# Optimization experiments

Hardware: AMD Instinct MI355X
Metric: run time of the kernel (lower is better)

The kernel has to match this reference:

```python
import jax, jax.numpy as jnp
import numpy as np

BS, S, E, H = 64, 512, 1024, 16
HD = E // H
MASK_ID, KNOW_ID = 30001, 30002


def setup_inputs() -> dict:
    key = jax.random.key(0)
    ks = jax.random.split(key, 8)
    model_output = jax.random.normal(ks[0], (BS, S, E), dtype=jnp.float32)
    ids = jax.random.randint(ks[1], (BS, S), 0, 30000)  # never hits special ids
    ids = ids.at[:, 0].set(MASK_ID)        # exactly one [MASK] per sequence
    ids = ids.at[:, 1:9].set(KNOW_ID)      # 8 knowledge slots per sequence
    knowledge_output = jax.random.normal(ks[2], (BS, E), dtype=jnp.float32)
    empty_knowledge_mask = jax.random.randint(ks[3], (BS,), 0, 2).astype(bool)
    bound = 1.0 / np.sqrt(E)
    in_proj_weight = jax.random.uniform(ks[4], (3 * E, E), minval=-bound, maxval=bound, dtype=jnp.float32)
    in_proj_bias = jnp.zeros((3 * E,), jnp.float32)
    out_proj_weight = jax.random.uniform(ks[5], (E, E), minval=-bound, maxval=bound, dtype=jnp.float32)
    out_proj_bias = jnp.zeros((E,), jnp.float32)
    attention_strength = jnp.float32(0.1)
    return {
        "model_output": model_output,
        "knowledge_output": knowledge_output,
        "in_proj_weight": in_proj_weight,
        "in_proj_bias": in_proj_bias,
        "out_proj_weight": out_proj_weight,
        "out_proj_bias": out_proj_bias,
        "attention_strength": attention_strength,
        "input_ids": ids,
        "empty_knowledge_mask": empty_knowledge_mask,
        "knowledge_token_id": KNOW_ID,
        "mask_token_id": MASK_ID,
    }


def reference(model_output, knowledge_output, in_proj_weight, in_proj_bias,
              out_proj_weight, out_proj_bias, attention_strength,
              input_ids, empty_knowledge_mask, knowledge_token_id, mask_token_id):
    bs, sent_len, hidden = model_output.shape
    # --- knowledge injection: scatter knowledge vector into knowledge-token slots ---
    knowledge_mask = input_ids == knowledge_token_id                 # [bs, S]
    kv_src = jnp.where(knowledge_mask[:, :, None],
                       knowledge_output[:, None, :], model_output)  # [bs, S, E]
    # --- single-query gather: one [MASK] position per sequence ---
    mask_pos = jnp.argmax(input_ids == mask_token_id, axis=1)        # [bs]
    q_in = jnp.take_along_axis(kv_src, mask_pos[:, None, None], axis=1)[:, 0, :]  # [bs, E]
    # --- nn.MultiheadAttention (eval mode, dropout=0) ---
    Wq, Wk, Wv = in_proj_weight[:E], in_proj_weight[E:2 * E], in_proj_weight[2 * E:]
    bq, bk, bv = in_proj_bias[:E], in_proj_bias[E:2 * E], in_proj_bias[2 * E:]
    q = (q_in @ Wq.T + bq).reshape(bs, H, HD)                        # [bs, H, hd]
    k = (kv_src @ Wk.T + bk).reshape(bs, sent_len, H, HD)            # [bs, S, H, hd]
    v = (kv_src @ Wv.T + bv).reshape(bs, sent_len, H, HD)
    scale = 1.0 / np.sqrt(HD)
    scores = jnp.einsum('bhd,bshd->bhs', q * scale, k)               # [bs, H, S]
    attn = jax.nn.softmax(scores, axis=-1)
    ctx = jnp.einsum('bhs,bshd->bhd', attn, v).reshape(bs, hidden)   # [bs, E]
    attn_output = ctx @ out_proj_weight.T + out_proj_bias            # [bs, E]
    # --- residual on the ORIGINAL (pre-injection) mask-token states ---
    origin_q = jnp.take_along_axis(model_output, mask_pos[:, None, None], axis=1)[:, 0, :]
    mask_output = origin_q + attention_strength * attn_output
    # --- conditional restore where knowledge is empty ---
    mask_output = jnp.where(empty_knowledge_mask[:, None], origin_q, mask_output)
    return mask_output
```

## Files before the change

### kernel.cpp

```cpp
#include <hip/hip_runtime.h>

#define BS 64
#define S  512
#define E  1024
#define H  16
#define HD 64
#define SCALE 0.125f
#define CATT 8

#define W_QIN  1024
#define W_QKBF 66560
#define W_NUM  1115136
#define W_DEN  9503744
#define W_CTX  9511936

typedef __attribute__((ext_vector_type(8))) short short8;
typedef __attribute__((ext_vector_type(4))) float floatx4;

__device__ __forceinline__ unsigned int pack_bf16(float a, float b) {
    unsigned int ua = __float_as_uint(a), ub = __float_as_uint(b);
    ua = (ua + 0x7fffu + ((ua >> 16) & 1u)) >> 16;
    ub = (ub + 0x7fffu + ((ub >> 16) & 1u)) >> 16;
    return ua | (ub << 16);
}

__device__ __forceinline__ void fma4(float4& acc, float s, const float4& v) {
    acc.x += s * v.x; acc.y += s * v.y; acc.z += s * v.z; acc.w += s * v.w;
}
__device__ __forceinline__ float dot4(const float4& a, const float4& b) {
    return a.x * b.x + a.y * b.y + a.z * b.z + a.w * b.w;
}
__device__ __forceinline__ void bfly8(float* a) {
    #pragma unroll
    for (int off = 32; off > 0; off >>= 1) {
        #pragma unroll
        for (int i = 0; i < 8; i++) a[i] += __shfl_xor(a[i], off, 64);
    }
}

__global__ void k_prep(const float* __restrict__ model, const float* __restrict__ knowledge,
                       const int* __restrict__ ids, const int* __restrict__ mask_id_p,
                       const int* __restrict__ kid_p, int* __restrict__ mp,
                       float* __restrict__ qin) {
    int b = blockIdx.x, tid = threadIdx.x;
    __shared__ int best;
    if (tid == 0) best = S;
    __syncthreads();
    int mid = mask_id_p[0];
    for (int s = tid; s < S; s += 256)
        if (ids[b * S + s] == mid) atomicMin(&best, s);
    __syncthreads();
    int m = (best == S) ? 0 : best;
    if (tid == 0) mp[b] = m;
    bool isk = (ids[b * S + m] == kid_p[0]);
    const float* qrow = isk ? knowledge + (size_t)b * E : model + ((size_t)(b * S + m)) * E;
    ((float4*)(qin + (size_t)b * E))[tid] = ((const float4*)qrow)[tid];
}

__global__ void k_qgen(const float* __restrict__ qin, const float* __restrict__ w_in,
                       const float* __restrict__ b_in, unsigned short* __restrict__ qkbf) {
    int h = blockIdx.x, b0 = blockIdx.y * 4, t = threadIdx.x;
    __shared__ float qin_l[4][1024];
    __shared__ float qred[4][64][4];
    __shared__ float qs_l[4][64];
    #pragma unroll
    for (int k = 0; k < 4; k++) {
        int idx4 = k * 256 + t;
        int bb = idx4 >> 8, col = (idx4 & 255) * 4;
        *(float4*)&qin_l[bb][col] = *(const float4*)(qin + (size_t)(b0 + bb) * E + col);
    }
    __syncthreads();
    {
        int d = t >> 2, part = t & 3;
        const float* wr = w_in + (size_t)(h * HD + d) * E + part * 256;
        float acc[4] = {0.f, 0.f, 0.f, 0.f};
        for (int i = 0; i < 64; i++) {
            float4 wv = *(const float4*)(wr + i * 4);
            #pragma unroll
            for (int bb = 0; bb < 4; bb++)
                acc[bb] += dot4(wv, *(const float4*)&qin_l[bb][part * 256 + i * 4]);
        }
        #pragma unroll
        for (int bb = 0; bb < 4; bb++) qred[bb][d][part] = acc[bb];
    }
    __syncthreads();
    if (t < 64) {
        float bias = b_in[h * HD + t];
        #pragma unroll
        for (int bb = 0; bb < 4; bb++)
            qs_l[bb][t] = qred[bb][t][0] + qred[bb][t][1] + qred[bb][t][2] + qred[bb][t][3] + bias;
    }
    __syncthreads();
    {
        int e0 = t * 4;
        const float* wk = w_in + (size_t)(E + h * HD) * E + e0;
        float4 acc[4];
        #pragma unroll
        for (int bb = 0; bb < 4; bb++) acc[bb] = make_float4(0.f, 0.f, 0.f, 0.f);
        for (int d = 0; d < HD; d++) {
            float4 wv = *(const float4*)(wk + (size_t)d * E);
            #pragma unroll
            for (int bb = 0; bb < 4; bb++) fma4(acc[bb], qs_l[bb][d], wv);
        }
        #pragma unroll
        for (int bb = 0; bb < 4; bb++) {
            uint2 pk;
            pk.x = pack_bf16(acc[bb].x * SCALE, acc[bb].y * SCALE);
            pk.y = pack_bf16(acc[bb].z * SCALE, acc[bb].w * SCALE);
            *(uint2*)&qkbf[((size_t)(b0 + bb) * H + h) * E + e0] = pk;
        }
    }
}

__global__ __launch_bounds__(512, 4) void k_attn(
    const float* __restrict__ model, const float* __restrict__ knowledge,
    const int* __restrict__ ids, const int* __restrict__ kid_p,
    const unsigned short* __restrict__ qkbf, float* __restrict__ num, float* __restrict__ den) {
    __shared__ unsigned short Rbuf[16 * 1032];
    __shared__ unsigned short Pbuf[16 * 40];
    __shared__ const float* rowp[64];
    int tid = threadIdx.x;
    int l = tid & 63, w = tid >> 6;
    int quad = l >> 4, lm = l & 15;
    int c = blockIdx.x, b = blockIdx.y;
    int s0 = c * 64;
    if (tid < 64) {
        int id = ids[b * S + s0 + tid];
        rowp[tid] = (id == kid_p[0]) ? knowledge + (size_t)b * E
                                     : model + ((size_t)(b * S + s0 + tid)) * E;
    }
    const unsigned short* qh = qkbf + ((size_t)b * H + lm) * E;
    floatx4 accn[8];
    #pragma unroll
    for (int i = 0; i < 8; i++) accn[i] = (floatx4)0.f;
    float accden = 0.f;
    int ebw = w * 8;
    __syncthreads();

    for (int pass = 0; pass < 4; pass++) {
        int rbase = pass * 16;
        #pragma unroll
        for (int k = 0; k < 8; k++) {
            int row = 2 * k + (tid >> 8);
            const float* rp = rowp[rbase + row];
            int col = (tid & 255) * 4;
            float4 v = *(const float4*)(rp + col);
            uint2 pk;
            pk.x = pack_bf16(v.x, v.y);
            pk.y = pack_bf16(v.z, v.w);
            *(uint2*)&Rbuf[row * 1032 + col] = pk;
        }
        __syncthreads();
        if (w == 0) {
            floatx4 accs = (floatx4)0.f;
            for (int kk = 0; kk < 32; kk++) {
                short8 a = *(const short8*)(const void*)&Rbuf[lm * 1032 + kk * 32 + quad * 8];
                short8 bf = *(const short8*)(const void*)(qh + kk * 32 + quad * 8);
                accs = __builtin_amdgcn_mfma_f32_16x16x32_bf16(a, bf, accs, 0, 0, 0);
            }
            float e0 = __expf(accs[0]), e1 = __expf(accs[1]);
            float e2 = __expf(accs[2]), e3 = __expf(accs[3]);
            float sum = e0 + e1 + e2 + e3;
            sum += __shfl_xor(sum, 16, 64);
            sum += __shfl_xor(sum, 32, 64);
            accden += sum;
            uint2 pw;
            pw.x = pack_bf16(e0, e1);
            pw.y = pack_bf16(e2, e3);
            *(uint2*)&Pbuf[lm * 40 + quad * 4] = pw;
        }
        __syncthreads();
        short8 afr = {};
        if (quad < 2) afr = *(const short8*)(const void*)&Pbuf[lm * 40 + quad * 8];
        #pragma unroll
        for (int i = 0; i < 8; i++) {
            int e = (ebw + i) * 16 + lm;
            short8 bfr = {};
            if (quad < 2) {
                #pragma unroll
                for (int j = 0; j < 8; j++)
                    bfr[j] = (short)Rbuf[(quad * 8 + j) * 1032 + e];
            }
            accn[i] = __builtin_amdgcn_mfma_f32_16x16x32_bf16(afr, bfr, accn[i], 0, 0, 0);
        }
        __syncthreads();
    }
    size_t base = ((size_t)(c * BS + b) * H) * E;
    #pragma unroll
    for (int i = 0; i < 8; i++) {
        int e = (ebw + i) * 16 + lm;
        num[base + (size_t)(quad * 4 + 0) * E + e] = accn[i][0];
        num[base + (size_t)(quad * 4 + 1) * E + e] = accn[i][1];
        num[base + (size_t)(quad * 4 + 2) * E + e] = accn[i][2];
        num[base + (size_t)(quad * 4 + 3) * E + e] = accn[i][3];
    }
    if (w == 0 && l < 16) den[(size_t)(c * BS + b) * H + l] = accden;
}

__global__ void k_pc(const float* __restrict__ num, const float* __restrict__ den,
                     const float* __restrict__ w_in, const float* __restrict__ b_in,
                     float* __restrict__ ctx) {
    int h = blockIdx.x, b0 = blockIdx.y * 4, t = threadIdx.x;
    __shared__ float p_l[4][1024];
    __shared__ float cred[4][64][4];
    __shared__ float inv_l[4];
    #pragma unroll
    for (int k = 0; k < 4; k++) {
        int idx4 = k * 256 + t;
        int bb = idx4 >> 8, e4 = (idx4 & 255) * 4;
        float4 a = make_float4(0.f, 0.f, 0.f, 0.f);
        for (int cc = 0; cc < CATT; cc++) {
            float4 v = *(const float4*)(num + (((size_t)(cc * BS + b0 + bb) * H + h) * E) + e4);
            a.x += v.x; a.y += v.y; a.z += v.z; a.w += v.w;
        }
        *(float4*)&p_l[bb][e4] = a;
    }
    if (t < 4) {
        float ds = 0.f;
        for (int cc = 0; cc < CATT; cc++) ds += den[(size_t)(cc * BS + b0 + t) * H + h];
        inv_l[t] = 1.0f / ds;
    }
    __syncthreads();
    {
        int jj = t >> 2, part = t & 3;
        const float* wr = w_in + (size_t)(2 * E + h * HD + jj) * E + part * 256;
        float acc[4] = {0.f, 0.f, 0.f, 0.f};
        for (int i = 0; i < 64; i++) {
            float4 wv = *(const float4*)(wr + i * 4);
            #pragma unroll
            for (int bb = 0; bb < 4; bb++)
                acc[bb] += dot4(wv, *(const float4*)&p_l[bb][part * 256 + i * 4]);
        }
        #pragma unroll
        for (int bb = 0; bb < 4; bb++) cred[bb][jj][part] = acc[bb];
    }
    __syncthreads();
    if (t < 64) {
        float bias = b_in[2 * E + h * HD + t];
        #pragma unroll
        for (int bb = 0; bb < 4; bb++) {
            float s = cred[bb][t][0] + cred[bb][t][1] + cred[bb][t][2] + cred[bb][t][3];
            ctx[(size_t)(b0 + bb) * E + h * HD + t] = inv_l[bb] * s + bias;
        }
    }
}

__global__ void k_out(const float* __restrict__ model, const float* __restrict__ w_out,
                      const float* __restrict__ b_out, const float* __restrict__ ctx,
                      const int* __restrict__ mp, const int* __restrict__ empty,
                      const float* __restrict__ strength_p, float* __restrict__ out) {
    int w = threadIdx.x >> 6, l = threadIdx.x & 63;
    int j = blockIdx.x * 4 + w;
    int b0 = blockIdx.y * 8;
    const float* wr = w_out + (size_t)j * E;
    float4 wv[4];
    #pragma unroll
    for (int r = 0; r < 4; r++) wv[r] = *(const float4*)(wr + r * 256 + l * 4);
    float acc[8];
    #pragma unroll
    for (int bb = 0; bb < 8; bb++) {
        const float* src = ctx + (size_t)(b0 + bb) * E;
        float a = 0.f;
        #pragma unroll
        for (int r = 0; r < 4; r++) a += dot4(wv[r], *(const float4*)(src + r * 256 + l * 4));
        acc[bb] = a;
    }
    bfly8(acc);
    if (l < 8) {
        float myacc = acc[0];
        #pragma unroll
        for (int bb = 1; bb < 8; bb++) myacc = (l == bb) ? acc[bb] : myacc;
        int b = b0 + l;
        int m = mp[b];
        float orig = model[((size_t)(b * S + m)) * E + j];
        float bias = b_out[j];
        float st = strength_p[0];
        out[(size_t)b * E + j] = empty[b] ? orig : orig + st * (myacc + bias);
    }
}

extern "C" void kernel_launch(void* const* d_in, const int* in_sizes, int n_in,
                              void* d_out, int out_size, void* d_ws, size_t ws_size,
                              hipStream_t stream) {
    const float* model     = (const float*)d_in[0];
    const float* knowledge = (const float*)d_in[1];
    const float* w_in      = (const float*)d_in[2];
    const float* b_in      = (const float*)d_in[3];
    const float* w_out     = (const float*)d_in[4];
    const float* b_out     = (const float*)d_in[5];
    const float* strength  = (const float*)d_in[6];
    const int*   ids       = (const int*)d_in[7];
    const int*   empty     = (const int*)d_in[8];
    const int*   know_id   = (const int*)d_in[9];
    const int*   mask_id   = (const int*)d_in[10];
    float* out = (float*)d_out;

    float* ws  = (float*)d_ws;
    int*   mp  = (int*)d_ws;
    float* qin = ws + W_QIN;
    unsigned short* qkbf = (unsigned short*)(ws + W_QKBF);
    float* num = ws + W_NUM;
    float* den = ws + W_DEN;
    float* ctx = ws + W_CTX;

    k_prep<<<BS, 256, 0, stream>>>(model, knowledge, ids, mask_id, know_id, mp, qin);
    k_qgen<<<dim3(H, 16), 256, 0, stream>>>(qin, w_in, b_in, qkbf);
    k_attn<<<dim3(CATT, BS), 512, 0, stream>>>(model, knowledge, ids, know_id, qkbf, num, den);
    k_pc<<<dim3(H, 16), 256, 0, stream>>>(num, den, w_in, b_in, ctx);
    k_out<<<dim3(256, 8), 256, 0, stream>>>(model, w_out, b_out, ctx, mp, empty, strength, out);
}
```

Measured before the change: 284.1 us.

## Split score MFMA across waves, add transposed LDS tile, coalesce num stores

The attention kernel now builds both a row-major bf16 tile and a transposed copy in LDS so the P·V MFMA B-fragments load as two 8-byte reads instead of eight strided scalar reads. The QK score reduction is spread over four waves with a shared-memory partial-sum reduction instead of one wave doing all 32 MFMAs. Knowledge-row selection uses a ballot bitmask instead of a pointer table, and numerator results are staged through LDS to be written with coalesced float4 stores. This costs much more LDS per block, which may reduce occupancy, and the global loads become scalar per thread rather than float4.

```diff
diff --git a/kernel.cpp b/kernel.cpp
--- a/kernel.cpp
+++ b/kernel.cpp
@@ -17,13 +17,15 @@
 typedef __attribute__((ext_vector_type(8))) short short8;
 typedef __attribute__((ext_vector_type(4))) float floatx4;
 
+union S8u { uint2 u2[2]; short8 s; };
+
+__device__ __forceinline__ unsigned short bf16c(float x) {
+    unsigned int u = __float_as_uint(x);
+    return (unsigned short)((u + 0x7fffu + ((u >> 16) & 1u)) >> 16);
+}
 __device__ __forceinline__ unsigned int pack_bf16(float a, float b) {
-    unsigned int ua = __float_as_uint(a), ub = __float_as_uint(b);
-    ua = (ua + 0x7fffu + ((ua >> 16) & 1u)) >> 16;
-    ub = (ub + 0x7fffu + ((ub >> 16) & 1u)) >> 16;
-    return ua | (ub << 16);
-}
-
+    return (unsigned int)bf16c(a) | ((unsigned int)bf16c(b) << 16);
+}
 __device__ __forceinline__ void fma4(float4& acc, float s, const float4& v) {
     acc.x += s * v.x; acc.y += s * v.y; acc.z += s * v.z; acc.w += s * v.w;
 }
@@ -116,57 +118,89 @@
     const float* __restrict__ model, const float* __restrict__ knowledge,
     const int* __restrict__ ids, const int* __restrict__ kid_p,
     const unsigned short* __restrict__ qkbf, float* __restrict__ num, float* __restrict__ den) {
-    __shared__ unsigned short Rbuf[16 * 1032];
+    __shared__ __align__(16) unsigned char Ubuf[73984];
+    unsigned short* Rbuf  = (unsigned short*)Ubuf;
+    unsigned short* RbufT = (unsigned short*)(Ubuf + 33024);
+    float* Tbuf = (float*)Ubuf;
     __shared__ unsigned short Pbuf[16 * 40];
-    __shared__ const float* rowp[64];
+    __shared__ float Sred[4][16][17];
+    __shared__ unsigned long long kmask_s;
+
     int tid = threadIdx.x;
-    int l = tid & 63, w = tid >> 6;
+    int w = tid >> 6, l = tid & 63;
     int quad = l >> 4, lm = l & 15;
     int c = blockIdx.x, b = blockIdx.y;
     int s0 = c * 64;
-    if (tid < 64) {
-        int id = ids[b * S + s0 + tid];
-        rowp[tid] = (id == kid_p[0]) ? knowledge + (size_t)b * E
-                                     : model + ((size_t)(b * S + s0 + tid)) * E;
-    }
-    const unsigned short* qh = qkbf + ((size_t)b * H + lm) * E;
+
+    if (w == 0) {
+        int id = ids[b * S + s0 + l];
+        unsigned long long mk = __ballot(id == kid_p[0]);
+        if (l == 0) kmask_s = mk;
+    }
     floatx4 accn[8];
     #pragma unroll
     for (int i = 0; i < 8; i++) accn[i] = (floatx4)0.f;
     float accden = 0.f;
-    int ebw = w * 8;
-    __syncthreads();
+    const float* kb = knowledge + (size_t)b * E;
+    const float* mb = model + (size_t)b * S * E;
+    const unsigned short* qh = qkbf + ((size_t)b * H + lm) * E;
+    __syncthreads();
+    unsigned long long kmask = kmask_s;
 
     for (int pass = 0; pass < 4; pass++) {
-        int rbase = pass * 16;
-        #pragma unroll
-        for (int k = 0; k < 8; k++) {
-            int row = 2 * k + (tid >> 8);
-            const float* rp = rowp[rbase + row];
-            int col = (tid & 255) * 4;
-            float4 v = *(const float4*)(rp + col);
-            uint2 pk;
-            pk.x = pack_bf16(v.x, v.y);
-            pk.y = pack_bf16(v.z, v.w);
-            *(uint2*)&Rbuf[row * 1032 + col] = pk;
+        int rb = pass * 16;
+        #pragma unroll
+        for (int g = 0; g < 4; g++) {
+            int r0 = g * 4;
+            const float* rp0 = ((kmask >> (rb + r0 + 0)) & 1ull) ? kb : mb + (size_t)(s0 + rb + r0 + 0) * E;
+            const float* rp1 = ((kmask >> (rb + r0 + 1)) & 1ull) ? kb : mb + (size_t)(s0 + rb + r0 + 1) * E;
+            const float* rp2 = ((kmask >> (rb + r0 + 2)) & 1ull) ? kb : mb + (size_t)(s0 + rb + r0 + 2) * E;
+            const float* rp3 = ((kmask >> (rb + r0 + 3)) & 1ull) ? kb : mb + (size_t)(s0 + rb + r0 + 3) * E;
+            #pragma unroll
+            for (int cc = 0; cc < 2; cc++) {
+                int col = cc * 512 + tid;
+                unsigned short h0 = bf16c(rp0[col]);
+                unsigned short h1 = bf16c(rp1[col]);
+                unsigned short h2 = bf16c(rp2[col]);
+                unsigned short h3 = bf16c(rp3[col]);
+                Rbuf[(r0 + 0) * 1032 + col] = h0;
+                Rbuf[(r0 + 1) * 1032 + col] = h1;
+                Rbuf[(r0 + 2) * 1032 + col] = h2;
+                Rbuf[(r0 + 3) * 1032 + col] = h3;
+                uint2 pk;
+                pk.x = (unsigned int)h0 | ((unsigned int)h1 << 16);
+                pk.y = (unsigned int)h2 | ((unsigned int)h3 << 16);
+                *(uint2*)&RbufT[col * 20 + r0] = pk;
+            }
+        }
+        __syncthreads();
+        if (w < 4) {
+            floatx4 acs = (floatx4)0.f;
+            #pragma unroll
+            for (int t = 0; t < 8; t++) {
+                int kk = w * 8 + t;
+                short8 a  = *(const short8*)(const void*)&Rbuf[lm * 1032 + kk * 32 + quad * 8];
+                short8 bf = *(const short8*)(const void*)(qh + kk * 32 + quad * 8);
+                acs = __builtin_amdgcn_mfma_f32_16x16x32_bf16(a, bf, acs, 0, 0, 0);
+            }
+            Sred[w][quad * 4 + 0][lm] = acs[0];
+            Sred[w][quad * 4 + 1][lm] = acs[1];
+            Sred[w][quad * 4 + 2][lm] = acs[2];
+            Sred[w][quad * 4 + 3][lm] = acs[3];
         }
         __syncthreads();
         if (w == 0) {
-            floatx4 accs = (floatx4)0.f;
-            for (int kk = 0; kk < 32; kk++) {
-                short8 a = *(const short8*)(const void*)&Rbuf[lm * 1032 + kk * 32 + quad * 8];
-                short8 bf = *(const short8*)(const void*)(qh + kk * 32 + quad * 8);
-                accs = __builtin_amdgcn_mfma_f32_16x16x32_bf16(a, bf, accs, 0, 0, 0);
+            float ex[4];
+            #pragma unroll
+            for (int r = 0; r < 4; r++) {
+                int row = quad * 4 + r;
+                float s = Sred[0][row][lm] + Sred[1][row][lm] + Sred[2][row][lm] + Sred[3][row][lm];
+                ex[r] = __expf(s);
+                accden += ex[r];
             }
-            float e0 = __expf(accs[0]), e1 = __expf(accs[1]);
-            float e2 = __expf(accs[2]), e3 = __expf(accs[3]);
-            float sum = e0 + e1 + e2 + e3;
-            sum += __shfl_xor(sum, 16, 64);
-            sum += __shfl_xor(sum, 32, 64);
-            accden += sum;
             uint2 pw;
-            pw.x = pack_bf16(e0, e1);
-            pw.y = pack_bf16(e2, e3);
+            pw.x = (unsigned int)bf16c(ex[0]) | ((unsigned int)bf16c(ex[1]) << 16);
+            pw.y = (unsigned int)bf16c(ex[2]) | ((unsigned int)bf16c(ex[3]) << 16);
             *(uint2*)&Pbuf[lm * 40 + quad * 4] = pw;
         }
         __syncthreads();
@@ -174,27 +208,37 @@
         if (quad < 2) afr = *(const short8*)(const void*)&Pbuf[lm * 40 + quad * 8];
         #pragma unroll
         for (int i = 0; i < 8; i++) {
-            int e = (ebw + i) * 16 + lm;
-            short8 bfr = {};
+            int e = (w * 8 + i) * 16 + lm;
+            S8u bb; bb.s = (short8){};
             if (quad < 2) {
-                #pragma unroll
-                for (int j = 0; j < 8; j++)
-                    bfr[j] = (short)Rbuf[(quad * 8 + j) * 1032 + e];
+                bb.u2[0] = *(const uint2*)&RbufT[e * 20 + quad * 8];
+                bb.u2[1] = *(const uint2*)&RbufT[e * 20 + quad * 8 + 4];
             }
-            accn[i] = __builtin_amdgcn_mfma_f32_16x16x32_bf16(afr, bfr, accn[i], 0, 0, 0);
+            accn[i] = __builtin_amdgcn_mfma_f32_16x16x32_bf16(afr, bb.s, accn[i], 0, 0, 0);
         }
         __syncthreads();
     }
+    #pragma unroll
+    for (int i = 0; i < 8; i++) {
+        int e = (w * 8 + i) * 16 + lm;
+        Tbuf[(quad * 4 + 0) * 1028 + e] = accn[i][0];
+        Tbuf[(quad * 4 + 1) * 1028 + e] = accn[i][1];
+        Tbuf[(quad * 4 + 2) * 1028 + e] = accn[i][2];
+        Tbuf[(quad * 4 + 3) * 1028 + e] = accn[i][3];
+    }
+    if (w == 0) {
+        accden += __shfl_xor(accden, 16, 64);
+        accden += __shfl_xor(accden, 32, 64);
+        if (l < 16) den[(size_t)(c * BS + b) * H + l] = accden;
+    }
+    __syncthreads();
     size_t base = ((size_t)(c * BS + b) * H) * E;
     #pragma unroll
-    for (int i = 0; i < 8; i++) {
-        int e = (ebw + i) * 16 + lm;
-        num[base + (size_t)(quad * 4 + 0) * E + e] = accn[i][0];
-        num[base + (size_t)(quad * 4 + 1) * E + e] = accn[i][1];
-        num[base + (size_t)(quad * 4 + 2) * E + e] = accn[i][2];
-        num[base + (size_t)(quad * 4 + 3) * E + e] = accn[i][3];
-    }
-    if (w == 0 && l < 16) den[(size_t)(c * BS + b) * H + l] = accden;
+    for (int k = 0; k < 8; k++) {
+        int idx4 = k * 512 + tid;
+        int h = idx4 >> 8, e4 = (idx4 & 255) * 4;
+        *(float4*)(num + base + (size_t)idx4 * 4) = *(const float4*)&Tbuf[h * 1028 + e4];
+    }
 }
 
 __global__ void k_pc(const float* __restrict__ num, const float* __restrict__ den,
```

After: 280.9 us. Within noise of the previous version (-1.1%).
